# Kernel tuning notes

Hardware: AMD Instinct MI355X
Metric: run time of the kernel (lower is better)

The kernel has to match this reference:

```python
import math
import jax, jax.numpy as jnp
import numpy as np


def positional_encoding(c, h, w):
    # Faithful port of the torch positional_encode grid (c divisible by 4).
    half = c // 2
    div = jnp.exp(jnp.arange(0, half, 2, dtype=jnp.float32) * (-math.log(10000.0) / half))  # [half/2]
    pos_w = jnp.arange(w, dtype=jnp.float32)[:, None]  # [w,1]
    pos_h = jnp.arange(h, dtype=jnp.float32)[:, None]  # [h,1]
    q = half // 2
    pe = jnp.zeros((c, h, w), dtype=jnp.float32)
    sw = jnp.sin(pos_w * div).T[:, None, :]  # [q,1,w] -> broadcast over height
    cw = jnp.cos(pos_w * div).T[:, None, :]
    sh = jnp.sin(pos_h * div).T[:, :, None]  # [q,h,1] -> broadcast over width
    ch = jnp.cos(pos_h * div).T[:, :, None]
    pe = pe.at[0:half:2].set(jnp.broadcast_to(sw, (q, h, w)))
    pe = pe.at[1:half:2].set(jnp.broadcast_to(cw, (q, h, w)))
    pe = pe.at[half::2].set(jnp.broadcast_to(sh, (q, h, w)))
    pe = pe.at[half + 1::2].set(jnp.broadcast_to(ch, (q, h, w)))
    return pe


def setup_inputs() -> dict:
    key = jax.random.key(0)
    k1, k2, k3, k4 = jax.random.split(key, 4)
    b, c, h, w = 4, 256, 64, 64
    x = jax.random.normal(k1, (b, c, h, w), dtype=jnp.float32)
    # kaiming_uniform-ish scale for d x d weights
    bound = 1.0 / math.sqrt(c)
    Wq = jax.random.uniform(k2, (c, c), dtype=jnp.float32, minval=-bound, maxval=bound)
    Wk = jax.random.uniform(k3, (c, c), dtype=jnp.float32, minval=-bound, maxval=bound)
    Wv = jax.random.uniform(k4, (c, c), dtype=jnp.float32, minval=-bound, maxval=bound)
    return {"x": x, "Wq": Wq, "Wk": Wk, "Wv": Wv}


def reference(x, Wq, Wk, Wv):
    b, c, h, w = x.shape
    pe = positional_encoding(c, h, w)
    xt = (x + pe).reshape(b, c, h * w).transpose(0, 2, 1)  # [b, hw, c]
    Q = xt @ Wq  # [b, hw, c]
    K = xt @ Wk
    V = xt @ Wv
    scores = jnp.einsum('bqc,bkc->bqk', Q, K) / math.sqrt(c)  # [b, hw, hw]
    # NOTE: softmax over dim=1 (the QUERY axis), matching nn.Softmax(dim=1)
    A = jax.nn.softmax(scores, axis=1)
    out = jnp.einsum('bqk,bkc->bqc', A, V)  # [b, hw, c]
    return out.transpose(0, 2, 1).reshape(b, c, h, w)
```

## Files before the change

kernel.cpp:

```cpp
#include <hip/hip_runtime.h>
#include <hip/hip_bf16.h>
#include <math.h>

typedef float f32x4 __attribute__((ext_vector_type(4)));
typedef short bf16x8 __attribute__((ext_vector_type(8)));
typedef short bf16x4 __attribute__((ext_vector_type(4)));

#define AS1 __attribute__((address_space(1)))
#define AS3 __attribute__((address_space(3)))

__device__ __forceinline__ short f2bf(float f) {
    unsigned u = __float_as_uint(f);
    unsigned r = (u + 0x7fffu + ((u >> 16) & 1u)) >> 16;
    return (short)r;
}
__device__ __forceinline__ float bf2f(short s) {
    return __uint_as_float(((unsigned)(unsigned short)s) << 16);
}
__device__ __forceinline__ void gld16(const void* g, void* l) {
    __builtin_amdgcn_global_load_lds((const AS1 unsigned int*)g, (AS3 unsigned int*)l, 16, 0, 0);
}

__device__ __forceinline__ void stage128x64(const short* __restrict__ g,
                                            short* lds, int t) {
    int w = t >> 6, l = t & 63;
    #pragma unroll
    for (int j = 0; j < 4; ++j) {
        int ii = j * 4 + w;
        int row = ii * 8 + (l >> 3);
        int slot = (l & 7) ^ (row & 7);
        gld16(g + row * 256 + slot * 8, lds + ii * 512);
    }
}

__device__ __forceinline__ void stage64x64(const short* __restrict__ g,
                                           short* lds, int t) {
    #pragma unroll
    for (int j = 0; j < 2; ++j) {
        int idx = j * 256 + t;
        int row = idx >> 3;
        int slot = (idx & 7) ^ (row & 7);
        gld16(g + (size_t)row * 4096 + slot * 8, lds + idx * 8);
    }
}

__device__ __forceinline__ void stage128x64v(const short* __restrict__ g,
                                             short* lds, int t) {
    #pragma unroll
    for (int j = 0; j < 4; ++j) {
        int idx = j * 256 + t;
        int row = idx >> 3;
        int slot = (idx & 7) ^ (row & 7);
        gld16(g + (size_t)row * 4096 + slot * 8, lds + idx * 8);
    }
}

__global__ void k_wt(const float* __restrict__ Wq, const float* __restrict__ Wk,
                     const float* __restrict__ Wv, short* __restrict__ Wt) {
    int bidx = blockIdx.x;
    int wsel = bidx >> 8, n = bidx & 255, k = threadIdx.x;
    const float* W = (wsel == 0) ? Wq : (wsel == 1) ? Wk : Wv;
    Wt[(wsel * 256 + n) * 256 + k] = f2bf(W[k * 256 + n]);
}

__global__ __launch_bounds__(256) void k_pe_xt(const float* __restrict__ x,
                                               short* __restrict__ xt) {
    int bid = blockIdx.x;
    int b = bid >> 7;
    int pb = bid & 127;
    __shared__ __align__(16) float tile[256][33];
    __shared__ __align__(16) float pew[128][32];
    __shared__ __align__(16) float peh[128];
    int t = threadIdx.x;
    const float c1 = 0.14391156f;
    int wbase = (pb & 1) * 32;
    int hpos = pb >> 1;
    #pragma unroll
    for (int j = 0; j < 16; ++j) {
        int idx = t + j * 256;
        int c = idx >> 5, pp = idx & 31;
        int i = c >> 1;
        float d = expf(-(float)i * c1);
        float arg = (float)(wbase + pp) * d;
        pew[c][pp] = (c & 1) ? cosf(arg) : sinf(arg);
    }
    if (t < 128) {
        int i = t >> 1;
        float d = expf(-(float)i * c1);
        float arg = (float)hpos * d;
        peh[t] = (t & 1) ? cosf(arg) : sinf(arg);
    }
    int p0 = pb * 32;
    #pragma unroll
    for (int j = 0; j < 32; ++j) {
        int c = j * 8 + (t >> 5);
        int pp = t & 31;
        tile[c][pp] = x[((b * 256 + c) << 12) + p0 + pp];
    }
    __syncthreads();
    int pp = t >> 3, cseg = t & 7;
    int p = p0 + pp;
    short* dst = xt + (((b << 12) + p) << 8) + (cseg << 5);
    #pragma unroll
    for (int j = 0; j < 4; ++j) {
        bf16x8 v;
        #pragma unroll
        for (int e = 0; e < 8; ++e) {
            int c = cseg * 32 + j * 8 + e;
            float pe = (c < 128) ? pew[c][pp] : peh[c - 128];
            v[e] = f2bf(tile[c][pp] + pe);
        }
        ((bf16x8*)dst)[j] = v;
    }
}

__global__ __launch_bounds__(256) void k_proj(const short* __restrict__ xt,
                                              const short* __restrict__ Wt,
                                              short* __restrict__ Q,
                                              short* __restrict__ K,
                                              short* __restrict__ VT) {
    int id = blockIdx.x;
    int wsel = id % 3; id /= 3;
    int nt = id & 1;  id >>= 1;
    int mt = id & 31; int b = id >> 5;
    int t = threadIdx.x, l = t & 63, w = t >> 6;
    int lr = l & 15, lg = l >> 4;
    int m0 = mt * 128 + (w >> 1) * 64;
    int n0 = nt * 128 + (w & 1) * 64;
    const short* wbase = Wt + wsel * 65536;
    f32x4 acc[4][4] = {};
    #pragma unroll
    for (int s = 0; s < 8; ++s) {
        bf16x8 af[4], bw[4];
        #pragma unroll
        for (int ms = 0; ms < 4; ++ms)
            af[ms] = *(const bf16x8*)(xt + ((b << 12) + m0 + ms * 16 + lr) * 256 + s * 32 + lg * 8);
        #pragma unroll
        for (int fn = 0; fn < 4; ++fn)
            bw[fn] = *(const bf16x8*)(wbase + (n0 + fn * 16 + lr) * 256 + s * 32 + lg * 8);
        #pragma unroll
        for (int ms = 0; ms < 4; ++ms)
            #pragma unroll
            for (int fn = 0; fn < 4; ++fn)
                acc[ms][fn] = __builtin_amdgcn_mfma_f32_16x16x32_bf16(af[ms], bw[fn], acc[ms][fn], 0, 0, 0);
    }
    if (wsel < 2) {
        float scl = (wsel == 0) ? 0.0625f : 1.0f;
        short* dst = (wsel == 0) ? Q : K;
        #pragma unroll
        for (int ms = 0; ms < 4; ++ms)
            #pragma unroll
            for (int fn = 0; fn < 4; ++fn)
                #pragma unroll
                for (int r = 0; r < 4; ++r) {
                    int m = m0 + ms * 16 + lg * 4 + r;
                    int n = n0 + fn * 16 + lr;
                    dst[((b << 12) + m) * 256 + n] = f2bf(acc[ms][fn][r] * scl);
                }
    } else {
        #pragma unroll
        for (int ms = 0; ms < 4; ++ms)
            #pragma unroll
            for (int fn = 0; fn < 4; ++fn) {
                int n = n0 + fn * 16 + lr;
                int m = m0 + ms * 16 + lg * 4;
                bf16x4 v;
                #pragma unroll
                for (int r = 0; r < 4; ++r) v[r] = f2bf(acc[ms][fn][r]);
                *(bf16x4*)(VT + ((b * 256 + n) << 12) + m) = v;
            }
    }
}

__global__ __launch_bounds__(256) void k_E(const short* __restrict__ Qm,
                                           const short* __restrict__ Km,
                                           short* __restrict__ E,
                                           float* __restrict__ pl) {
    int o = blockIdx.x;
    int bid = (o & 7) * 512 + (o >> 3);
    int qt = bid & 31, kt = (bid >> 5) & 31, b = bid >> 10;
    int t = threadIdx.x, l = t & 63;
    int w = t >> 6;
    int wr = w >> 1, wc = w & 1;
    int lr = l & 15, lg = l >> 4;
    __shared__ __align__(16) short Ka[128 * 64];
    __shared__ __align__(16) short Qa[128 * 64];
    __shared__ float plds[128];
    const short* Kg = Km + (((size_t)b << 12) + kt * 128) * 256;
    const short* Qg = Qm + (((size_t)b << 12) + qt * 128) * 256;
    f32x4 acc[4][4] = {};

    #pragma unroll
    for (int ks = 0; ks < 4; ++ks) {
        stage128x64(Kg + ks * 64, Ka, t);
        stage128x64(Qg + ks * 64, Qa, t);
        __syncthreads();
        #pragma unroll
        for (int s = 0; s < 2; ++s) {
            bf16x8 a[4], bq[4];
            #pragma unroll
            for (int mk = 0; mk < 4; ++mk) {
                int row = wr * 64 + mk * 16 + lr;
                a[mk] = *(const bf16x8*)(Ka + row * 64 + (((s * 4 + lg) ^ (row & 7)) << 3));
            }
            #pragma unroll
            for (int nq = 0; nq < 4; ++nq) {
                int row = wc * 64 + nq * 16 + lr;
                bq[nq] = *(const bf16x8*)(Qa + row * 64 + (((s * 4 + lg) ^ (row & 7)) << 3));
            }
            #pragma unroll
            for (int mk = 0; mk < 4; ++mk)
                #pragma unroll
                for (int nq = 0; nq < 4; ++nq)
                    acc[mk][nq] = __builtin_amdgcn_mfma_f32_16x16x32_bf16(a[mk], bq[nq], acc[mk][nq], 0, 0, 0);
        }
        __syncthreads();
    }

    int k0 = kt * 128 + wr * 64;
    int q0 = qt * 128 + wc * 64;
    float psum[4][4];
    #pragma unroll
    for (int mk = 0; mk < 4; ++mk) {
        float ps0 = 0.f, ps1 = 0.f, ps2 = 0.f, ps3 = 0.f;
        #pragma unroll
        for (int nq = 0; nq < 4; ++nq) {
            int q = q0 + nq * 16 + lr;
            float e0 = __expf(acc[mk][nq][0]);
            float e1 = __expf(acc[mk][nq][1]);
            float e2 = __expf(acc[mk][nq][2]);
            float e3 = __expf(acc[mk][nq][3]);
            ps0 += e0; ps1 += e1; ps2 += e2; ps3 += e3;
            bf16x4 ev;
            ev[0] = f2bf(e0); ev[1] = f2bf(e1); ev[2] = f2bf(e2); ev[3] = f2bf(e3);
            *(bf16x4*)(E + (((size_t)b << 12) + q) * 4096 + k0 + mk * 16 + lg * 4) = ev;
        }
        psum[mk][0] = ps0; psum[mk][1] = ps1; psum[mk][2] = ps2; psum[mk][3] = ps3;
    }
    #pragma unroll
    for (int mk = 0; mk < 4; ++mk)
        #pragma unroll
        for (int r = 0; r < 4; ++r) {
            float v = psum[mk][r];
            v += __shfl_xor(v, 1);
            v += __shfl_xor(v, 2);
            v += __shfl_xor(v, 4);
            v += __shfl_xor(v, 8);
            psum[mk][r] = v;
        }
    if (wc == 0 && lr == 0) {
        #pragma unroll
        for (int mk = 0; mk < 4; ++mk)
            #pragma unroll
            for (int r = 0; r < 4; ++r)
                plds[wr * 64 + mk * 16 + lg * 4 + r] = psum[mk][r];
    }
    __syncthreads();
    if (wc == 1 && lr == 0) {
        #pragma unroll
        for (int mk = 0; mk < 4; ++mk)
            #pragma unroll
            for (int r = 0; r < 4; ++r)
                plds[wr * 64 + mk * 16 + lg * 4 + r] += psum[mk][r];
    }
    __syncthreads();
    if (t < 128) pl[(b * 32 + qt) * 4096 + kt * 128 + t] = plds[t];
}

__global__ void k_lred(const float* __restrict__ pl, float* __restrict__ rl) {
    int gid = blockIdx.x * 256 + threadIdx.x;
    float s = 0.f;
    int b = gid >> 12, k = gid & 4095;
    #pragma unroll
    for (int qt = 0; qt < 32; ++qt) s += pl[(b * 32 + qt) * 4096 + k];
    rl[gid] = 1.0f / s;
}

__global__ void k_vn(const short* __restrict__ VT, const float* __restrict__ rl,
                     short* __restrict__ Vnt) {
    int gid = blockIdx.x * 256 + threadIdx.x;
    int idx8 = gid * 8;
    int b = idx8 >> 20;
    int rem = idx8 & 1048575;
    int k = rem & 4095;
    bf16x8 v = *(const bf16x8*)(VT + idx8);
    const float* rb = rl + (b << 12) + k;
    f32x4 r0 = *(const f32x4*)(rb);
    f32x4 r1 = *(const f32x4*)(rb + 4);
    bf16x8 oo;
    #pragma unroll
    for (int e = 0; e < 8; ++e) {
        float f = bf2f(v[e]);
        float rr = (e < 4) ? r0[e] : r1[e - 4];
        oo[e] = f2bf(f * rr);
    }
    *(bf16x8*)(Vnt + idx8) = oo;
}

__global__ __launch_bounds__(256) void k_pv(const short* __restrict__ E,
                                            const short* __restrict__ Vnt,
                                            float* __restrict__ out) {
    int o = blockIdx.x;
    int ct = o >> 8;
    int r = o & 255;
    int b = r >> 6, qt = r & 63;
    int t = threadIdx.x, l = t & 63, w = t >> 6;
    int wq = w >> 1, wc = w & 1;
    int lr = l & 15, lg = l >> 4;
    int q0 = qt * 64, c0 = ct * 128;
    __shared__ __align__(16) short Ea[64 * 64];
    __shared__ __align__(16) short Va[128 * 64];
    const short* Eg = E + (((size_t)b << 12) + q0) * 4096;
    const short* Vg = Vnt + ((size_t)(b * 256 + c0)) * 4096;
    f32x4 acc[2][4] = {};

    for (int kc = 0; kc < 4096; kc += 64) {
        stage64x64(Eg + kc, Ea, t);
        stage128x64v(Vg + kc, Va, t);
        __syncthreads();
        bf16x8 Af[2][2], Bf[4][2];
        #pragma unroll
        for (int s = 0; s < 2; ++s) {
            #pragma unroll
            for (int mq = 0; mq < 2; ++mq) {
                int row = wq * 32 + mq * 16 + lr;
                Af[mq][s] = *(const bf16x8*)(Ea + row * 64 + (((s * 4 + lg) ^ (row & 7)) << 3));
            }
            #pragma unroll
            for (int nc = 0; nc < 4; ++nc) {
                int row = wc * 64 + nc * 16 + lr;
                Bf[nc][s] = *(const bf16x8*)(Va + row * 64 + (((s * 4 + lg) ^ (row & 7)) << 3));
            }
        }
        #pragma unroll
        for (int s = 0; s < 2; ++s)
            #pragma unroll
            for (int mq = 0; mq < 2; ++mq)
                #pragma unroll
                for (int nc = 0; nc < 4; ++nc)
                    acc[mq][nc] = __builtin_amdgcn_mfma_f32_16x16x32_bf16(Af[mq][s], Bf[nc][s], acc[mq][nc], 0, 0, 0);
        __syncthreads();
    }
    #pragma unroll
    for (int mq = 0; mq < 2; ++mq)
        #pragma unroll
        for (int nc = 0; nc < 4; ++nc) {
            int c = c0 + wc * 64 + nc * 16 + lr;
            int q = q0 + wq * 32 + mq * 16 + lg * 4;
            *(f32x4*)(out + (((size_t)b << 8) + c) * 4096 + q) = acc[mq][nc];
        }
}

extern "C" void kernel_launch(void* const* d_in, const int* in_sizes, int n_in,
                              void* d_out, int out_size, void* d_ws, size_t ws_size,
                              hipStream_t stream) {
    const float* x  = (const float*)d_in[0];
    const float* Wq = (const float*)d_in[1];
    const float* Wk = (const float*)d_in[2];
    const float* Wv = (const float*)d_in[3];

    char* p = (char*)d_ws;
    short* xt  = (short*)p; p += 4 * 4096 * 256 * 2;
    short* Wt  = (short*)p; p += 3 * 256 * 256 * 2;
    short* Qm  = (short*)p; p += 4 * 4096 * 256 * 2;
    short* Km  = (short*)p; p += 4 * 4096 * 256 * 2;
    short* VT  = (short*)p; p += 4 * 4096 * 256 * 2;
    short* E   = (short*)p; p += (size_t)4 * 4096 * 4096 * 2;
    float* pl  = (float*)p; p += 4 * 32 * 4096 * 4;
    float* rl  = (float*)p; p += 4 * 4096 * 4;
    short* Vnt = (short*)p; p += 4 * 4096 * 256 * 2;

    float* out = (float*)d_out;

    k_wt   <<<768, 256, 0, stream>>>(Wq, Wk, Wv, Wt);
    k_pe_xt<<<512, 256, 0, stream>>>(x, xt);
    k_proj <<<768, 256, 0, stream>>>(xt, Wt, Qm, Km, VT);
    k_E    <<<4096, 256, 0, stream>>>(Qm, Km, E, pl);
    k_lred <<<64,   256, 0, stream>>>(pl, rl);
    k_vn   <<<2048, 256, 0, stream>>>(VT, rl, Vnt);
    k_pv   <<<512,  256, 0, stream>>>(E, Vnt, out);
}
```

Measured before the change: 178.7 us.

## Merge prep kernels and make k_E process two key tiles with software prefetch

The weight-transpose and positional-encoding kernels are fused into one launch to save a kernel launch. k_E now handles two consecutive key tiles per block, halving the grid. It issues the next K/Q slice loads right after the compute barrier so they overlap the following work, and the first tile's exp/store epilogue overlaps the second tile's staging. This adds an occupancy hint of 4 blocks per CU and reloads the same Q slices for the second tile, trading extra register pressure for fewer launches and better latency hiding.

```diff
diff --git a/kernel.cpp b/kernel.cpp
--- a/kernel.cpp
+++ b/kernel.cpp
@@ -55,17 +55,20 @@
     }
 }
 
-__global__ void k_wt(const float* __restrict__ Wq, const float* __restrict__ Wk,
-                     const float* __restrict__ Wv, short* __restrict__ Wt) {
+__global__ __launch_bounds__(256) void k_prep(const float* __restrict__ x,
+                                              const float* __restrict__ Wq,
+                                              const float* __restrict__ Wk,
+                                              const float* __restrict__ Wv,
+                                              short* __restrict__ xt,
+                                              short* __restrict__ Wt) {
     int bidx = blockIdx.x;
-    int wsel = bidx >> 8, n = bidx & 255, k = threadIdx.x;
-    const float* W = (wsel == 0) ? Wq : (wsel == 1) ? Wk : Wv;
-    Wt[(wsel * 256 + n) * 256 + k] = f2bf(W[k * 256 + n]);
-}
-
-__global__ __launch_bounds__(256) void k_pe_xt(const float* __restrict__ x,
-                                               short* __restrict__ xt) {
-    int bid = blockIdx.x;
+    if (bidx < 768) {
+        int wsel = bidx >> 8, n = bidx & 255, k = threadIdx.x;
+        const float* W = (wsel == 0) ? Wq : (wsel == 1) ? Wk : Wv;
+        Wt[(wsel * 256 + n) * 256 + k] = f2bf(W[k * 256 + n]);
+        return;
+    }
+    int bid = bidx - 768;
     int b = bid >> 7;
     int pb = bid & 127;
     __shared__ __align__(16) float tile[256][33];
@@ -172,51 +175,12 @@
     }
 }
 
-__global__ __launch_bounds__(256) void k_E(const short* __restrict__ Qm,
-                                           const short* __restrict__ Km,
-                                           short* __restrict__ E,
-                                           float* __restrict__ pl) {
-    int o = blockIdx.x;
-    int bid = (o & 7) * 512 + (o >> 3);
-    int qt = bid & 31, kt = (bid >> 5) & 31, b = bid >> 10;
-    int t = threadIdx.x, l = t & 63;
-    int w = t >> 6;
+__device__ __forceinline__ void k_E_fin(f32x4 (&acc)[4][4], short* __restrict__ E,
+                                        float* __restrict__ pl, float* plds,
+                                        int b, int qt, int kt, int t) {
+    int l = t & 63, w = t >> 6;
     int wr = w >> 1, wc = w & 1;
     int lr = l & 15, lg = l >> 4;
-    __shared__ __align__(16) short Ka[128 * 64];
-    __shared__ __align__(16) short Qa[128 * 64];
-    __shared__ float plds[128];
-    const short* Kg = Km + (((size_t)b << 12) + kt * 128) * 256;
-    const short* Qg = Qm + (((size_t)b << 12) + qt * 128) * 256;
-    f32x4 acc[4][4] = {};
-
-    #pragma unroll
-    for (int ks = 0; ks < 4; ++ks) {
-        stage128x64(Kg + ks * 64, Ka, t);
-        stage128x64(Qg + ks * 64, Qa, t);
-        __syncthreads();
-        #pragma unroll
-        for (int s = 0; s < 2; ++s) {
-            bf16x8 a[4], bq[4];
-            #pragma unroll
-            for (int mk = 0; mk < 4; ++mk) {
-                int row = wr * 64 + mk * 16 + lr;
-                a[mk] = *(const bf16x8*)(Ka + row * 64 + (((s * 4 + lg) ^ (row & 7)) << 3));
-            }
-            #pragma unroll
-            for (int nq = 0; nq < 4; ++nq) {
-                int row = wc * 64 + nq * 16 + lr;
-                bq[nq] = *(const bf16x8*)(Qa + row * 64 + (((s * 4 + lg) ^ (row & 7)) << 3));
-            }
-            #pragma unroll
-            for (int mk = 0; mk < 4; ++mk)
-                #pragma unroll
-                for (int nq = 0; nq < 4; ++nq)
-                    acc[mk][nq] = __builtin_amdgcn_mfma_f32_16x16x32_bf16(a[mk], bq[nq], acc[mk][nq], 0, 0, 0);
-        }
-        __syncthreads();
-    }
-
     int k0 = kt * 128 + wr * 64;
     int q0 = qt * 128 + wc * 64;
     float psum[4][4];
@@ -265,6 +229,70 @@
     }
     __syncthreads();
     if (t < 128) pl[(b * 32 + qt) * 4096 + kt * 128 + t] = plds[t];
+}
+
+__global__ __launch_bounds__(256, 4) void k_E(const short* __restrict__ Qm,
+                                              const short* __restrict__ Km,
+                                              short* __restrict__ E,
+                                              float* __restrict__ pl) {
+    int o = blockIdx.x;
+    int bid = (o & 7) * 256 + (o >> 3);
+    int qt = bid & 31, ktp = (bid >> 5) & 15, b = bid >> 9;
+    int t = threadIdx.x, l = t & 63;
+    int w = t >> 6;
+    int wr = w >> 1, wc = w & 1;
+    int lr = l & 15, lg = l >> 4;
+    __shared__ __align__(16) short Ka[128 * 64];
+    __shared__ __align__(16) short Qa[128 * 64];
+    __shared__ float plds[128];
+    const short* Qg = Qm + (((size_t)b << 12) + qt * 128) * 256;
+    const short* Kg0 = Km + (((size_t)b << 12) + ktp * 256) * 256;
+    f32x4 acc[4][4] = {};
+
+    stage128x64(Kg0, Ka, t);
+    stage128x64(Qg, Qa, t);
+    #pragma unroll
+    for (int tile = 0; tile < 2; ++tile) {
+        const short* Kg = Kg0 + tile * (128 * 256);
+        #pragma unroll
+        for (int ks = 0; ks < 4; ++ks) {
+            __syncthreads();
+            #pragma unroll
+            for (int s = 0; s < 2; ++s) {
+                bf16x8 a[4], bq[4];
+                #pragma unroll
+                for (int mk = 0; mk < 4; ++mk) {
+                    int row = wr * 64 + mk * 16 + lr;
+                    a[mk] = *(const bf16x8*)(Ka + row * 64 + (((s * 4 + lg) ^ (row & 7)) << 3));
+                }
+                #pragma unroll
+                for (int nq = 0; nq < 4; ++nq) {
+                    int row = wc * 64 + nq * 16 + lr;
+                    bq[nq] = *(const bf16x8*)(Qa + row * 64 + (((s * 4 + lg) ^ (row & 7)) << 3));
+                }
+                #pragma unroll
+                for (int mk = 0; mk < 4; ++mk)
+                    #pragma unroll
+                    for (int nq = 0; nq < 4; ++nq)
+                        acc[mk][nq] = __builtin_amdgcn_mfma_f32_16x16x32_bf16(a[mk], bq[nq], acc[mk][nq], 0, 0, 0);
+            }
+            __syncthreads();
+            if (ks < 3) {
+                stage128x64(Kg + (ks + 1) * 64, Ka, t);
+                stage128x64(Qg + (ks + 1) * 64, Qa, t);
+            } else if (tile == 0) {
+                stage128x64(Kg0 + 128 * 256, Ka, t);
+                stage128x64(Qg, Qa, t);
+                k_E_fin(acc, E, pl, plds, b, qt, ktp * 2, t);
+                #pragma unroll
+                for (int mk = 0; mk < 4; ++mk)
+                    #pragma unroll
+                    for (int nq = 0; nq < 4; ++nq)
+                        acc[mk][nq] = (f32x4){0.f, 0.f, 0.f, 0.f};
+            }
+        }
+    }
+    k_E_fin(acc, E, pl, plds, b, qt, ktp * 2 + 1, t);
 }
 
 __global__ void k_lred(const float* __restrict__ pl, float* __restrict__ rl) {
@@ -372,10 +400,9 @@
 
     float* out = (float*)d_out;
 
-    k_wt   <<<768, 256, 0, stream>>>(Wq, Wk, Wv, Wt);
-    k_pe_xt<<<512, 256, 0, stream>>>(x, xt);
+    k_prep <<<1280, 256, 0, stream>>>(x, Wq, Wk, Wv, xt, Wt);
     k_proj <<<768, 256, 0, stream>>>(xt, Wt, Qm, Km, VT);
-    k_E    <<<4096, 256, 0, stream>>>(Qm, Km, E, pl);
+    k_E    <<<2048, 256, 0, stream>>>(Qm, Km, E, pl);
     k_lred <<<64,   256, 0, stream>>>(pl, rl);
     k_vn   <<<2048, 256, 0, stream>>>(VT, rl, Vnt);
     k_pv   <<<512,  256, 0, stream>>>(E, Vnt, out);
```

New measurement: 199.0 us. 1.11x slower.
